# Optimization experiments

Measured on AMD Instinct MI355X. Metric: run time of the kernel, lower is better.

Reference implementation:

```python
import jax, jax.numpy as jnp
import numpy as np

B, S, D, H = 2, 2048, 1024, 16
HD = D // H  # 64

def setup_inputs() -> dict:
    key = jax.random.key(0)
    k1, k2, k3 = jax.random.split(key, 3)
    hidden_states = jax.random.normal(k1, (B, S, D), dtype=jnp.float32)
    w_attn = jax.random.normal(k2, (D, 3 * D), dtype=jnp.float32) * 0.02
    w_proj = jax.random.normal(k3, (D, D), dtype=jnp.float32) * 0.02
    return {"hidden_states": hidden_states, "w_attn": w_attn, "w_proj": w_proj}

def reference(hidden_states, w_attn, w_proj):
    b, s, d = hidden_states.shape
    # c_attn: Conv1D (bias is a scalar zero in the source)
    qkv = jnp.einsum('bsd,de->bse', hidden_states, w_attn)  # [B,S,3D]
    q, k, v = jnp.split(qkv, 3, axis=-1)
    def split_heads(t):
        return t.reshape(b, s, H, HD).transpose(0, 2, 1, 3)  # [B,H,S,HD]
    q, k, v = split_heads(q), split_heads(k), split_heads(v)
    # eager attention; scale_attn_weights=True -> divide by sqrt(head_dim)
    scores = jnp.einsum('bhqd,bhkd->bhqk', q, k) / jnp.sqrt(jnp.float32(HD))
    # NOTE: source registers bias buffer as all-ones (True), so the causal
    # torch.where is a no-op -- faithfully no masking is applied.
    probs = jax.nn.softmax(scores, axis=-1)
    attn = jnp.einsum('bhqk,bhkd->bhqd', probs, v)  # [B,H,S,HD]
    attn = attn.transpose(0, 2, 1, 3).reshape(b, s, d)  # merge heads
    out = jnp.einsum('bsd,de->bse', attn, w_proj)  # c_proj (zero bias)
    return out
```

## Files before the change

### kernel.cpp

```cpp
#include <hip/hip_runtime.h>
#include <hip/hip_bf16.h>

typedef __attribute__((ext_vector_type(8))) short bf16x8;
typedef __attribute__((ext_vector_type(4))) short short4v;
typedef __attribute__((ext_vector_type(4))) float f32x4;
typedef __attribute__((ext_vector_type(16))) float f32x16;
typedef __attribute__((ext_vector_type(4))) float float4v;

__device__ __forceinline__ short f2bf(float f) {
    union { float f; unsigned u; } v; v.f = f;
    unsigned r = v.u + 0x7fffu + ((v.u >> 16) & 1u);
    return (short)(r >> 16);
}

__device__ __forceinline__ void gload16(const short* g, short* lds) {
    __builtin_amdgcn_global_load_lds(
        (const __attribute__((address_space(1))) unsigned*)g,
        (__attribute__((address_space(3))) unsigned*)lds, 16, 0, 0);
}

__global__ __launch_bounds__(256) void cvt_bf16x8(const float* __restrict__ in,
                                                  short* __restrict__ out) {
    int i = (blockIdx.x * 256 + threadIdx.x) * 8;
    float4v a0 = *reinterpret_cast<const float4v*>(&in[i]);
    float4v a1 = *reinterpret_cast<const float4v*>(&in[i + 4]);
    bf16x8 s;
    s[0] = f2bf(a0[0]); s[1] = f2bf(a0[1]); s[2] = f2bf(a0[2]); s[3] = f2bf(a0[3]);
    s[4] = f2bf(a1[0]); s[5] = f2bf(a1[1]); s[6] = f2bf(a1[2]); s[7] = f2bf(a1[3]);
    *reinterpret_cast<bf16x8*>(&out[i]) = s;
}

__global__ __launch_bounds__(256) void tconv(const float* __restrict__ in,
                                             short* __restrict__ out,
                                             int Kdim, int Ndim) {
    __shared__ int Ls[64][65];
    const int t = threadIdx.x;
    const int k0 = blockIdx.y * 64, n0 = blockIdx.x * 64;
    const int kl = t >> 4, n4 = (t & 15) * 4;
#pragma unroll
    for (int it = 0; it < 4; ++it) {
        int k = kl + it * 16;
        float4v v = *reinterpret_cast<const float4v*>(&in[(size_t)(k0 + k) * Ndim + n0 + n4]);
#pragma unroll
        for (int c = 0; c < 4; ++c) Ls[k][n4 + c] = (int)(unsigned short)f2bf(v[c]);
    }
    __syncthreads();
    const int nl0 = t >> 4, kq = (t & 15) * 4;
#pragma unroll
    for (int it = 0; it < 4; ++it) {
        int nl = nl0 + it * 16;
        short4v s;
#pragma unroll
        for (int j = 0; j < 4; ++j) s[j] = (short)Ls[kq + j][nl];
        *reinterpret_cast<short4v*>(&out[(size_t)(n0 + nl) * Kdim + k0 + kq]) = s;
    }
}

__global__ __launch_bounds__(256) void qkv_gemm(const short* __restrict__ Ah,
                                                const short* __restrict__ Wt,
                                                short* __restrict__ Qw,
                                                short* __restrict__ Kw,
                                                short* __restrict__ Vt) {
    __shared__ short As[128 * 64];
    __shared__ short Bs[128 * 64];
    const int tid = threadIdx.x;
    const int l = tid & 63, w = tid >> 6;
    const int g = l >> 4, lr = l & 15;
    const int r8 = l >> 3, sl = l & 7;
    const int xs = (sl ^ r8) * 8;
    const int wm = (w >> 1) * 64, wn = (w & 1) * 64;
    const int m0 = blockIdx.y * 128;
    const int n0 = blockIdx.x * 128;
    f32x4 acc[4][4] = {};
    for (int k0 = 0; k0 < 1024; k0 += 64) {
        const short* Ag = Ah + m0 * 1024 + k0;
        const short* Bg = Wt + n0 * 1024 + k0;
#pragma unroll
        for (int i = 0; i < 4; ++i) {
            int seg = w * 4 + i;
            gload16(Ag + (seg * 8 + r8) * 1024 + xs, &As[seg * 512]);
            gload16(Bg + (seg * 8 + r8) * 1024 + xs, &Bs[seg * 512]);
        }
        __syncthreads();
#pragma unroll
        for (int kk = 0; kk < 2; ++kk) {
            bf16x8 af[4], bfr[4];
#pragma unroll
            for (int mi = 0; mi < 4; ++mi) {
                int row = wm + mi * 16 + lr;
                af[mi] = *reinterpret_cast<const bf16x8*>(&As[row * 64 + (((4 * kk + g) ^ (lr & 7)) * 8)]);
            }
#pragma unroll
            for (int ni = 0; ni < 4; ++ni) {
                int col = wn + ni * 16 + lr;
                bfr[ni] = *reinterpret_cast<const bf16x8*>(&Bs[col * 64 + (((4 * kk + g) ^ (lr & 7)) * 8)]);
            }
#pragma unroll
            for (int mi = 0; mi < 4; ++mi)
#pragma unroll
                for (int ni = 0; ni < 4; ++ni)
                    acc[mi][ni] = __builtin_amdgcn_mfma_f32_16x16x32_bf16(af[mi], bfr[ni], acc[mi][ni], 0, 0, 0);
        }
        __syncthreads();
    }
#pragma unroll
    for (int mi = 0; mi < 4; ++mi) {
        int m = m0 + wm + mi * 16 + g * 4;
        int bb = m >> 11, s0 = m & 2047;
#pragma unroll
        for (int ni = 0; ni < 4; ++ni) {
            int n = n0 + wn + ni * 16 + lr;
            int which = n >> 10, hh = (n >> 6) & 15, d = n & 63;
            if (which == 2) {
                short4v pv;
#pragma unroll
                for (int r = 0; r < 4; ++r) pv[r] = f2bf(acc[mi][ni][r]);
                *reinterpret_cast<short4v*>(&Vt[(((bb * 16 + hh) * 64) + d) * 2048 + s0]) = pv;
            } else {
                short* dst = which ? Kw : Qw;
                float sc = which ? 1.0f : 0.18033688011112042f;
#pragma unroll
                for (int r = 0; r < 4; ++r)
                    dst[((bb * 16 + hh) * 2048 + s0 + r) * 64 + d] = f2bf(acc[mi][ni][r] * sc);
            }
        }
    }
}

__global__ __launch_bounds__(128, 2) void attn6(const short* __restrict__ Qw,
                                                const short* __restrict__ Kw,
                                                const short* __restrict__ Vt,
                                                short* __restrict__ Ow) {
    __shared__ short Ks[2][64 * 64];
    __shared__ short Vs[2][64 * 64];
    const int tid = threadIdx.x;
    const int w = tid >> 6, l = tid & 63;
    const int q = l & 31, hi = l >> 5;
    const int r8 = l >> 3, sl = l & 7;
    const int xs = (sl ^ r8) * 8;
    const int bid = blockIdx.x;
    const int work = (bid & 7) * 128 + (bid >> 3);
    const int head = work >> 5, qblk = work & 31;
    const int b = head >> 4, h = head & 15;
    const int q0 = qblk * 64 + w * 32;
    const short* Qb = Qw + ((b * 16 + h) * 2048 + q0) * 64;
    const short* Kb = Kw + ((b * 16 + h) * 2048) * 64;
    const short* Vb = Vt + ((b * 16 + h) * 64) * 2048;

    bf16x8 qb[4];
#pragma unroll
    for (int c = 0; c < 4; ++c)
        qb[c] = *reinterpret_cast<const bf16x8*>(&Qb[q * 64 + c * 16 + hi * 8]);

    f32x16 o0 = {}, o1 = {};
    float psum = 0.f;

#define STAGE_KV(buf, j0)                                                        \
    {                                                                            \
        _Pragma("unroll")                                                        \
        for (int i = 0; i < 4; ++i) {                                            \
            int seg = w * 4 + i;                                                 \
            gload16(Kb + ((j0) + seg * 8 + r8) * 64 + xs, &Ks[buf][seg * 512]);  \
            gload16(Vb + (seg * 8 + r8) * 2048 + (j0) + xs, &Vs[buf][seg * 512]);\
        }                                                                        \
    }

    STAGE_KV(0, 0);
    __syncthreads();
    int cur = 0;

    for (int jt = 0; jt < 32; ++jt) {
        if (jt < 31) STAGE_KV(cur ^ 1, (jt + 1) * 64);

#pragma unroll
        for (int sub = 0; sub < 2; ++sub) {
            f32x16 st = {};
#pragma unroll
            for (int c = 0; c < 4; ++c) {
                bf16x8 ka = *reinterpret_cast<const bf16x8*>(
                    &Ks[cur][(sub * 32 + q) * 64 + (((2 * c + hi) ^ (q & 7)) * 8)]);
                st = __builtin_amdgcn_mfma_f32_32x32x16_bf16(ka, qb[c], st, 0, 0, 0);
            }
            float p[16];
#pragma unroll
            for (int r = 0; r < 16; ++r) p[r] = __builtin_amdgcn_exp2f(st[r]);
            float s01 = (p[0] + p[1]) + (p[2] + p[3]);
            float s23 = (p[4] + p[5]) + (p[6] + p[7]);
            float s45 = (p[8] + p[9]) + (p[10] + p[11]);
            float s67 = (p[12] + p[13]) + (p[14] + p[15]);
            psum += (s01 + s23) + (s45 + s67);
            int pk[4][2];
#pragma unroll
            for (int bq = 0; bq < 4; ++bq) {
                int w0, w1;
                asm("v_cvt_pk_bf16_f32 %0, %1, %2" : "=v"(w0) : "v"(p[4 * bq]), "v"(p[4 * bq + 1]));
                asm("v_cvt_pk_bf16_f32 %0, %1, %2" : "=v"(w1) : "v"(p[4 * bq + 2]), "v"(p[4 * bq + 3]));
                pk[bq][0] = w0; pk[bq][1] = w1;
            }
#pragma unroll
            for (int c2 = 0; c2 < 2; ++c2) {
                int w0 = pk[2 * c2][0], w2 = pk[2 * c2 + 1][0];
                int w1 = pk[2 * c2][1], w3 = pk[2 * c2 + 1][1];
                asm("v_permlane32_swap_b32 %0, %1" : "+v"(w0), "+v"(w2));
                asm("v_permlane32_swap_b32 %0, %1" : "+v"(w1), "+v"(w3));
                union { int wd[4]; bf16x8 v; } pb;
                pb.wd[0] = w0; pb.wd[1] = w1; pb.wd[2] = w2; pb.wd[3] = w3;
#pragma unroll
                for (int dt = 0; dt < 2; ++dt) {
                    bf16x8 va = *reinterpret_cast<const bf16x8*>(
                        &Vs[cur][(dt * 32 + q) * 64 + (((4 * sub + 2 * c2 + hi) ^ (q & 7)) * 8)]);
                    if (dt == 0) o0 = __builtin_amdgcn_mfma_f32_32x32x16_bf16(va, pb.v, o0, 0, 0, 0);
                    else         o1 = __builtin_amdgcn_mfma_f32_32x32x16_bf16(va, pb.v, o1, 0, 0, 0);
                }
            }
        }
        __syncthreads();
        cur ^= 1;
    }
#undef STAGE_KV

    int pa = __float_as_int(psum), pb2 = pa;
    asm("v_permlane32_swap_b32 %0, %1" : "+v"(pa), "+v"(pb2));
    float tot = __int_as_float(pa) + __int_as_float(pb2);
    float inv = 1.f / tot;

    short* Orow = &Ow[(b * 2048 + q0 + q) * 1024 + h * 64];
#pragma unroll
    for (int r = 0; r < 4; ++r) {
        short4v ov0, ov1;
#pragma unroll
        for (int j = 0; j < 4; ++j) {
            ov0[j] = f2bf(o0[4 * r + j] * inv);
            ov1[j] = f2bf(o1[4 * r + j] * inv);
        }
        *reinterpret_cast<short4v*>(&Orow[8 * r + 4 * hi]) = ov0;
        *reinterpret_cast<short4v*>(&Orow[32 + 8 * r + 4 * hi]) = ov1;
    }
}

__global__ __launch_bounds__(256) void proj_gemm(const short* __restrict__ Ag,
                                                 const short* __restrict__ Wtp,
                                                 float* __restrict__ Out) {
    __shared__ short As[128 * 64];
    __shared__ short Bs[128 * 64];
    const int tid = threadIdx.x;
    const int l = tid & 63, w = tid >> 6;
    const int g = l >> 4, lr = l & 15;
    const int r8 = l >> 3, sl = l & 7;
    const int xs = (sl ^ r8) * 8;
    const int wm = (w >> 1) * 64, wn = (w & 1) * 64;
    const int m0 = blockIdx.y * 128;
    const int n0 = blockIdx.x * 128;
    f32x4 acc[4][4] = {};
    for (int k0 = 0; k0 < 1024; k0 += 64) {
        const short* Ab = Ag + m0 * 1024 + k0;
        const short* Bg = Wtp + n0 * 1024 + k0;
#pragma unroll
        for (int i = 0; i < 4; ++i) {
            int seg = w * 4 + i;
            gload16(Ab + (seg * 8 + r8) * 1024 + xs, &As[seg * 512]);
            gload16(Bg + (seg * 8 + r8) * 1024 + xs, &Bs[seg * 512]);
        }
        __syncthreads();
#pragma unroll
        for (int kk = 0; kk < 2; ++kk) {
            bf16x8 af[4], bfr[4];
#pragma unroll
            for (int mi = 0; mi < 4; ++mi) {
                int row = wm + mi * 16 + lr;
                af[mi] = *reinterpret_cast<const bf16x8*>(&As[row * 64 + (((4 * kk + g) ^ (lr & 7)) * 8)]);
            }
#pragma unroll
            for (int ni = 0; ni < 4; ++ni) {
                int col = wn + ni * 16 + lr;
                bfr[ni] = *reinterpret_cast<const bf16x8*>(&Bs[col * 64 + (((4 * kk + g) ^ (lr & 7)) * 8)]);
            }
#pragma unroll
            for (int mi = 0; mi < 4; ++mi)
#pragma unroll
                for (int ni = 0; ni < 4; ++ni)
                    acc[mi][ni] = __builtin_amdgcn_mfma_f32_16x16x32_bf16(af[mi], bfr[ni], acc[mi][ni], 0, 0, 0);
        }
        __syncthreads();
    }
#pragma unroll
    for (int mi = 0; mi < 4; ++mi) {
#pragma unroll
        for (int ni = 0; ni < 4; ++ni) {
            int n = n0 + wn + ni * 16 + lr;
#pragma unroll
            for (int r = 0; r < 4; ++r) {
                int mm = m0 + wm + mi * 16 + g * 4 + r;
                Out[mm * 1024 + n] = acc[mi][ni][r];
            }
        }
    }
}

extern "C" void kernel_launch(void* const* d_in, const int* in_sizes, int n_in,
                              void* d_out, int out_size, void* d_ws, size_t ws_size,
                              hipStream_t stream) {
    const float* hidden = (const float*)d_in[0];
    const float* w_attn = (const float*)d_in[1];
    const float* w_proj = (const float*)d_in[2];
    float* out = (float*)d_out;

    short* AhOw = (short*)d_ws;
    short* Qw = AhOw + 4194304;
    short* Kw = Qw + 4194304;
    short* Vt = Kw + 4194304;
    short* Wta = (short*)d_out;

    cvt_bf16x8<<<dim3(2048), 256, 0, stream>>>(hidden, AhOw);
    tconv<<<dim3(48, 16), 256, 0, stream>>>(w_attn, Wta, 1024, 3072);
    qkv_gemm<<<dim3(24, 32), 256, 0, stream>>>(AhOw, Wta, Qw, Kw, Vt);
    attn6<<<dim3(1024), 128, 0, stream>>>(Qw, Kw, Vt, AhOw);
    tconv<<<dim3(16, 16), 256, 0, stream>>>(w_proj, Qw, 1024, 1024);
    proj_gemm<<<dim3(8, 32), 256, 0, stream>>>(AhOw, Qw, out);
}
```

Baseline: 140.1 us.

## Split attention over key halves with 4-wave blocks and add merge kernel

The attention kernel now splits the key sequence into two halves per block and runs 256-thread blocks covering 128 queries, each block staging only its 1024-key half. Partial normalized outputs and row sums go to two buffers, and a new merge kernel reweights and combines them. This cuts per-block serial loop length and raises the threads per block. In exchange it adds an extra bf16 round trip of partial outputs, a separate launch, and extra rounding from storing partials in bf16. Partials and sums are parked in spare regions of the output buffer.

```diff
diff --git a/kernel.cpp b/kernel.cpp
--- a/kernel.cpp
+++ b/kernel.cpp
@@ -11,6 +11,11 @@
     union { float f; unsigned u; } v; v.f = f;
     unsigned r = v.u + 0x7fffu + ((v.u >> 16) & 1u);
     return (short)(r >> 16);
+}
+__device__ __forceinline__ float bf2f(short s) {
+    union { unsigned u; float f; } v;
+    v.u = ((unsigned)(unsigned short)s) << 16;
+    return v.f;
 }
 
 __device__ __forceinline__ void gload16(const short* g, short* lds) {
@@ -127,10 +132,12 @@
     }
 }
 
-__global__ __launch_bounds__(128, 2) void attn6(const short* __restrict__ Qw,
-                                                const short* __restrict__ Kw,
-                                                const short* __restrict__ Vt,
-                                                short* __restrict__ Ow) {
+__global__ __launch_bounds__(256, 4) void attn6s(const short* __restrict__ Qw,
+                                                 const short* __restrict__ Kw,
+                                                 const short* __restrict__ Vt,
+                                                 short* __restrict__ N0,
+                                                 short* __restrict__ N1,
+                                                 float* __restrict__ Tot) {
     __shared__ short Ks[2][64 * 64];
     __shared__ short Vs[2][64 * 64];
     const int tid = threadIdx.x;
@@ -140,12 +147,14 @@
     const int xs = (sl ^ r8) * 8;
     const int bid = blockIdx.x;
     const int work = (bid & 7) * 128 + (bid >> 3);
-    const int head = work >> 5, qblk = work & 31;
+    const int head = work >> 5;
+    const int qblk = (work & 31) >> 1;
+    const int ks = work & 1;
     const int b = head >> 4, h = head & 15;
-    const int q0 = qblk * 64 + w * 32;
+    const int q0 = qblk * 128 + w * 32;
     const short* Qb = Qw + ((b * 16 + h) * 2048 + q0) * 64;
-    const short* Kb = Kw + ((b * 16 + h) * 2048) * 64;
-    const short* Vb = Vt + ((b * 16 + h) * 64) * 2048;
+    const short* Kb = Kw + ((b * 16 + h) * 2048 + ks * 1024) * 64;
+    const short* Vb = Vt + ((b * 16 + h) * 64) * 2048 + ks * 1024;
 
     bf16x8 qb[4];
 #pragma unroll
@@ -158,8 +167,8 @@
 #define STAGE_KV(buf, j0)                                                        \
     {                                                                            \
         _Pragma("unroll")                                                        \
-        for (int i = 0; i < 4; ++i) {                                            \
-            int seg = w * 4 + i;                                                 \
+        for (int i = 0; i < 2; ++i) {                                            \
+            int seg = w * 2 + i;                                                 \
             gload16(Kb + ((j0) + seg * 8 + r8) * 64 + xs, &Ks[buf][seg * 512]);  \
             gload16(Vb + (seg * 8 + r8) * 2048 + (j0) + xs, &Vs[buf][seg * 512]);\
         }                                                                        \
@@ -169,8 +178,8 @@
     __syncthreads();
     int cur = 0;
 
-    for (int jt = 0; jt < 32; ++jt) {
-        if (jt < 31) STAGE_KV(cur ^ 1, (jt + 1) * 64);
+    for (int jt = 0; jt < 16; ++jt) {
+        if (jt < 15) STAGE_KV(cur ^ 1, (jt + 1) * 64);
 
 #pragma unroll
         for (int sub = 0; sub < 2; ++sub) {
@@ -224,7 +233,8 @@
     float tot = __int_as_float(pa) + __int_as_float(pb2);
     float inv = 1.f / tot;
 
-    short* Orow = &Ow[(b * 2048 + q0 + q) * 1024 + h * 64];
+    short* Nd = ks ? N1 : N0;
+    short* Orow = &Nd[(b * 2048 + q0 + q) * 1024 + h * 64];
 #pragma unroll
     for (int r = 0; r < 4; ++r) {
         short4v ov0, ov1;
@@ -236,6 +246,26 @@
         *reinterpret_cast<short4v*>(&Orow[8 * r + 4 * hi]) = ov0;
         *reinterpret_cast<short4v*>(&Orow[32 + 8 * r + 4 * hi]) = ov1;
     }
+    if (hi == 0)
+        Tot[ks * 65536 + (b * 16 + h) * 2048 + q0 + q] = tot;
+}
+
+__global__ __launch_bounds__(256) void attn_merge(short* __restrict__ N0,
+                                                  const short* __restrict__ N1,
+                                                  const float* __restrict__ Tot) {
+    int i = (blockIdx.x * 256 + threadIdx.x) * 8;
+    int bs = i >> 10, h = (i >> 6) & 15;
+    int b = bs >> 11, s = bs & 2047;
+    int qi = (b * 16 + h) * 2048 + s;
+    float t0 = Tot[qi], t1 = Tot[65536 + qi];
+    float inv = 1.f / (t0 + t1);
+    float w0 = t0 * inv, w1 = t1 * inv;
+    bf16x8 a = *reinterpret_cast<const bf16x8*>(&N0[i]);
+    bf16x8 c = *reinterpret_cast<const bf16x8*>(&N1[i]);
+    bf16x8 r;
+#pragma unroll
+    for (int j = 0; j < 8; ++j) r[j] = f2bf(bf2f(a[j]) * w0 + bf2f(c[j]) * w1);
+    *reinterpret_cast<bf16x8*>(&N0[i]) = r;
 }
 
 __global__ __launch_bounds__(256) void proj_gemm(const short* __restrict__ Ag,
@@ -305,16 +335,19 @@
     const float* w_proj = (const float*)d_in[2];
     float* out = (float*)d_out;
 
-    short* AhOw = (short*)d_ws;
-    short* Qw = AhOw + 4194304;
+    short* AhN0 = (short*)d_ws;
+    short* Qw = AhN0 + 4194304;
     short* Kw = Qw + 4194304;
     short* Vt = Kw + 4194304;
     short* Wta = (short*)d_out;
-
-    cvt_bf16x8<<<dim3(2048), 256, 0, stream>>>(hidden, AhOw);
+    float* Tot = (float*)((char*)d_out + 7u * 1024 * 1024);
+    short* N1 = (short*)((char*)d_out + 8u * 1024 * 1024);
+
+    cvt_bf16x8<<<dim3(2048), 256, 0, stream>>>(hidden, AhN0);
     tconv<<<dim3(48, 16), 256, 0, stream>>>(w_attn, Wta, 1024, 3072);
-    qkv_gemm<<<dim3(24, 32), 256, 0, stream>>>(AhOw, Wta, Qw, Kw, Vt);
-    attn6<<<dim3(1024), 128, 0, stream>>>(Qw, Kw, Vt, AhOw);
+    qkv_gemm<<<dim3(24, 32), 256, 0, stream>>>(AhN0, Wta, Qw, Kw, Vt);
+    attn6s<<<dim3(1024), 256, 0, stream>>>(Qw, Kw, Vt, AhN0, N1, Tot);
+    attn_merge<<<dim3(2048), 256, 0, stream>>>(AhN0, N1, Tot);
     tconv<<<dim3(16, 16), 256, 0, stream>>>(w_proj, Qw, 1024, 1024);
-    proj_gemm<<<dim3(8, 32), 256, 0, stream>>>(AhOw, Qw, out);
-}
+    proj_gemm<<<dim3(8, 32), 256, 0, stream>>>(AhN0, Qw, out);
+}
```

Measured after the change: 135.0 us. 1.04x faster.
